# Performance work log

Hardware: AMD Instinct MI355X
Metric: run time of the kernel (lower is better)

## Reference

```python
import jax, jax.numpy as jnp
import numpy as np

N_ELEMENTS = 64  # StructureElementLayer(n_elements=64)


def setup_inputs() -> dict:
    key = jax.random.key(0)
    k1, k2 = jax.random.split(key)
    # x: [N, C, T, V] skeleton sequence (batch, coord channels, time, joints)
    x = jax.random.normal(k1, (256, 3, 256, 25), dtype=jnp.float32)
    # StructureElementLayer parameters (torch.rand init / ones*3 init)
    centres = jax.random.uniform(k2, (N_ELEMENTS, 2), dtype=jnp.float32)
    sharpness = jnp.ones((N_ELEMENTS, 2), dtype=jnp.float32) * 3.0
    return {"x": x, "centres": centres, "sharpness": sharpness}


def _mst_deaths(D):
    """Dim-0 Vietoris-Rips persistence deaths == MST edge weights (Prim's algorithm).

    D: [n, n] symmetric distance matrix. Returns [n-1] finite death values
    (births are all 0; the single essential (0, inf) pair contributes
    exp(-inf)=0 to the structure-element layer and is dropped).
    """
    n = D.shape[0]
    in_tree = jnp.zeros((n,), dtype=bool).at[0].set(True)
    dist = D[0]  # min distance from each node to the current tree

    def step(carry, _):
        in_tree, dist = carry
        d = jnp.where(in_tree, jnp.inf, dist)
        j = jnp.argmin(d)
        w = d[j]
        in_tree = in_tree.at[j].set(True)
        dist = jnp.minimum(dist, D[j])
        return (in_tree, dist), w

    (_, _), deaths = jax.lax.scan(step, (in_tree, dist), None, length=n - 1)
    return deaths


def _forward(x, centres, sharpness):
    xm = x.mean(1)                                  # [N, T, V]
    diff = xm[..., :, None] - xm[..., None, :]      # [N, T, V, V] pairwise joint diffs
    diff = diff.mean(-3)                            # [N, V, V]
    feat = jnp.linalg.norm(diff, axis=1)            # [N, V]  (torch.norm(., 2, dim=1))
    feat = (feat - feat.min()) / (feat.max() - feat.min())
    # Euclidean distance matrix of the N points in V-dim space (grad-safe sqrt)
    sq = jnp.sum(feat * feat, axis=1)
    D2 = sq[:, None] + sq[None, :] - 2.0 * (feat @ feat.T)
    D2 = jnp.maximum(D2, 0.0)
    D = jnp.where(D2 > 0.0, jnp.sqrt(jnp.where(D2 > 0.0, D2, 1.0)), 0.0)
    deaths = _mst_deaths(D)                         # [N-1]
    diag = jnp.stack([jnp.zeros_like(deaths), deaths], axis=-1)  # [N-1, 2] (birth, death)
    # StructureElementLayer: sum_i exp(-sum_d (p_id - c_kd)^2 * s_kd^2)
    d2 = (diag[:, None, :] - centres[None, :, :]) ** 2            # [N-1, K, 2]
    out = jnp.exp(-(d2 * (sharpness ** 2)).sum(-1)).sum(0)        # [K]
    return out


def reference(x, centres, sharpness):
    return _forward(x, centres, sharpness)
```

## Files before the change

### kernel.cpp

```cpp
#include <hip/hip_runtime.h>
#include <hip/hip_fp16.h>


#define WS_M    0
#define WS_MM   25600
#define WS_RK   28672
#define WS_D16  65536
#define WS_MP   196608

#define INF32 0xFFFFFFFFu
#define MPSTR 132

__global__ void k_mean(const float* __restrict__ x, float* __restrict__ m,
                       unsigned int* __restrict__ Mp) {
    const int n = blockIdx.x;
    const int tid = threadIdx.x;
    if (tid < 66) Mp[n * 66 + tid] = INF32;
    __shared__ float sums[25];
    if (tid < 25) sums[tid] = 0.0f;
    __syncthreads();
    if (tid < 200) {
        const float* base = x + (long)n * 19200 + 4 * tid;
        float a0 = 0.f, a1 = 0.f, a2 = 0.f, a3 = 0.f;
        #pragma unroll
        for (int i = 0; i < 24; ++i) {
            float4 v = *reinterpret_cast<const float4*>(base + 800 * i);
            a0 += v.x; a1 += v.y; a2 += v.z; a3 += v.w;
        }
        const int v0 = (4 * tid) % 25;
        atomicAdd(&sums[v0], a0);
        atomicAdd(&sums[(v0 + 1) % 25], a1);
        atomicAdd(&sums[(v0 + 2) % 25], a2);
        atomicAdd(&sums[(v0 + 3) % 25], a3);
    }
    __syncthreads();
    if (tid < 25) m[n * 25 + tid] = sums[tid] * (1.0f / 768.0f);
}

template <int CTRL>
__device__ __forceinline__ unsigned int dpp_min_step(unsigned int v) {
    unsigned int t = (unsigned int)__builtin_amdgcn_update_dpp(
        (int)0xFFFFFFFF, (int)v, CTRL, 0xF, 0xF, false);
    return (t < v) ? t : v;
}

__global__ void __launch_bounds__(256) k_dist(const float* __restrict__ m,
                                              unsigned short* __restrict__ D16,
                                              unsigned int* __restrict__ rowKeyG,
                                              unsigned int* __restrict__ mm) {
    __shared__ float mS[6400];
    __shared__ float featS[6400];
    __shared__ unsigned int bmin, bmax;
    __shared__ unsigned int wred[4];
    const int i = blockIdx.x;
    const int t = threadIdx.x;
    if (t == 0) { bmin = 0x7F800000u; bmax = 0u; }
    #pragma unroll
    for (int it = 0; it < 7; ++it) {
        int o = it * 256 + t;
        if (o < 1600) reinterpret_cast<float4*>(mS)[o] =
            reinterpret_cast<const float4*>(m)[o];
    }
    __syncthreads();
    float r[25];
    #pragma unroll
    for (int v = 0; v < 25; ++v) r[v] = mS[t * 25 + v];
    float S1 = 0.f, S2 = 0.f;
    #pragma unroll
    for (int v = 0; v < 25; ++v) { S1 += r[v]; S2 += r[v] * r[v]; }
    float fmn = 1e30f, fmx = -1e30f;
    #pragma unroll
    for (int w = 0; w < 25; ++w) {
        float q = S2 - 2.f * r[w] * S1 + 25.f * r[w] * r[w];
        q = fmaxf(q, 0.f);
        float f = sqrtf(q);
        featS[t * 25 + w] = f;
        fmn = fminf(fmn, f); fmx = fmaxf(fmx, f);
    }
    if (i == 0) {
        atomicMin(&bmin, __float_as_uint(fmn));
        atomicMax(&bmax, __float_as_uint(fmx));
    }
    __syncthreads();
    if (i == 0 && t == 0) { mm[0] = bmin; mm[1] = bmax; }
    float fi[25];
    #pragma unroll
    for (int v = 0; v < 25; ++v) fi[v] = featS[i * 25 + v];
    float s = 0.f;
    #pragma unroll
    for (int v = 0; v < 25; ++v) { float d = fi[v] - featS[t * 25 + v]; s += d * d; }
    const unsigned int w16 = (unsigned int)__half_as_ushort(__float2half(s));
    D16[i * 256 + t] = (unsigned short)w16;
    const unsigned int lo = (i < t) ? i : t, hi = (i < t) ? t : i;
    unsigned int key = (t == i) ? INF32 : ((w16 << 16) | (lo << 8) | hi);
    key = dpp_min_step<0x111>(key);
    key = dpp_min_step<0x112>(key);
    key = dpp_min_step<0x114>(key);
    key = dpp_min_step<0x118>(key);
    key = dpp_min_step<0x142>(key);
    key = dpp_min_step<0x143>(key);
    if ((t & 63) == 63) wred[t >> 6] = key;
    __syncthreads();
    if (t == 0) {
        unsigned int b0 = wred[0] < wred[1] ? wred[0] : wred[1];
        unsigned int b1 = wred[2] < wred[3] ? wred[2] : wred[3];
        rowKeyG[i] = b0 < b1 ? b0 : b1;
    }
}

template <bool RECORD>
__device__ __forceinline__ void wave0_phase(int n, int lane,
        unsigned int* rowKeyS, unsigned char* parentS, unsigned char* newidS,
        unsigned char* cmapS, float* deaths, unsigned int* ncS, unsigned int* dcS) {
    unsigned int par[4];
    #pragma unroll
    for (int s = 0; s < 4; ++s) {
        const int i = lane + 64 * s;
        if (i < n) {
            const unsigned int rk = rowKeyS[i];
            const unsigned int u = (rk >> 8) & 0xFFu, v = rk & 0xFFu;
            unsigned int p = (u == (unsigned int)i) ? v : u;
            if (rk == INF32) p = (unsigned int)i;
            par[s] = p;
            parentS[i] = (unsigned char)p;
        }
    }
    #pragma unroll
    for (int s = 0; s < 4; ++s) {
        const int i = lane + 64 * s;
        if (i < n) {
            const unsigned int p = par[s];
            if (p != (unsigned int)i) {
                if (parentS[p] == (unsigned char)i && (unsigned int)i < p) {
                    parentS[i] = (unsigned char)i;
                } else if (RECORD) {
                    const unsigned int d = atomicAdd(dcS, 1u);
                    const unsigned int rk = rowKeyS[i];
                    deaths[d] = sqrtf(__half2float(__ushort_as_half(
                        (unsigned short)(rk >> 16))));
                }
            }
        }
    }
    for (;;) {
        bool ch = false;
        #pragma unroll
        for (int s = 0; s < 4; ++s) {
            const int i = lane + 64 * s;
            if (i < n) {
                const unsigned char p0 = parentS[i];
                const unsigned char np = parentS[p0];
                if (np != p0) { ch = true; parentS[i] = np; }
            }
        }
        if (__ballot(ch) == 0ull) break;
    }
    bool isr[4];
    #pragma unroll
    for (int s = 0; s < 4; ++s) {
        const int i = lane + 64 * s;
        isr[s] = (i < n) && (parentS[i] == (unsigned char)i);
    }
    unsigned int base = 0;
    const unsigned long long below = (1ull << lane) - 1ull;
    #pragma unroll
    for (int s = 0; s < 4; ++s) {
        const unsigned long long mask = __ballot(isr[s]);
        if (isr[s]) {
            const int i = lane + 64 * s;
            newidS[i] = (unsigned char)(base + __popcll(mask & below));
        }
        base += (unsigned int)__popcll(mask);
    }
    if (lane == 0) *ncS = base;
    #pragma unroll
    for (int s = 0; s < 4; ++s) {
        const int i = lane + 64 * s;
        if (i < n) cmapS[i] = newidS[parentS[i]];
    }
}

__global__ void __launch_bounds__(256) k_contract(const unsigned short* __restrict__ D16g,
                                                  const unsigned int* __restrict__ rowKeyG,
                                                  unsigned int* __restrict__ Mp) {
    __shared__ unsigned int rowKeyS[256];
    __shared__ unsigned char parentS[256], newidS[256], cmapS[256];
    __shared__ unsigned int ncS;
    const int tid = threadIdx.x;
    const int b = blockIdx.x;
    rowKeyS[tid] = rowKeyG[tid];
    __syncthreads();
    if (tid < 64)
        wave0_phase<false>(256, tid, rowKeyS, parentS, newidS, cmapS,
                           nullptr, &ncS, nullptr);
    __syncthreads();
    const unsigned int ca = cmapS[b];
    const unsigned int cb = cmapS[tid];
    if (ca != cb) {
        const unsigned int w16 = (unsigned int)D16g[b * 256 + tid];
        const unsigned int lo = ca < cb ? ca : cb;
        const unsigned int hi = ca < cb ? cb : ca;
        atomicMin(&Mp[ca * MPSTR + cb], (w16 << 16) | (lo << 8) | hi);
    }
}

#define SA 132
#define SB 68
#define OFF_B (128 * SA)

__global__ void __launch_bounds__(1024) k_mst(const unsigned int* __restrict__ Mp,
                                              const unsigned int* __restrict__ rowKeyG,
                                              const unsigned int* __restrict__ mm,
                                              const float* __restrict__ centres,
                                              const float* __restrict__ sharp,
                                              float* __restrict__ out) {
    __shared__ unsigned int Mb[128 * SA + 64 * SB];
    __shared__ unsigned int rowKeyS[256];
    __shared__ unsigned char parentS[256], newidS[256], cmapS[256];
    __shared__ unsigned int ncS, dcS;
    __shared__ float deaths[256];
    __shared__ float outpart[1024];
    const int tid = threadIdx.x;

    if (tid < 256) rowKeyS[tid] = rowKeyG[tid];
    if (tid == 0) dcS = 0;
    __syncthreads();
    if (tid < 64)
        wave0_phase<true>(256, tid, rowKeyS, parentS, newidS, cmapS,
                          deaths, &ncS, &dcS);
    __syncthreads();
    int n = (int)ncS;

    for (int idx = tid; idx < n * SA; idx += 1024) Mb[idx] = Mp[idx];
    __syncthreads();

    int srcOff = 0, srcStr = SA, dstOff = OFF_B, dstStr = SB;
    for (int round = 0; round < 12 && n > 1; ++round) {
        if (tid < n) rowKeyS[tid] = INF32;
        __syncthreads();
        if (tid < 8 * n) {
            const int a = tid >> 3, sub = tid & 7;
            const unsigned int* row = &Mb[srcOff + a * srcStr];
            unsigned int best = INF32;
            for (int b2 = sub; b2 < n; b2 += 8) {
                const unsigned int v = row[b2];
                best = v < best ? v : best;
            }
            if (best != INF32) atomicMin(&rowKeyS[a], best);
        }
        __syncthreads();
        if (tid < 64)
            wave0_phase<true>(n, tid, rowKeyS, parentS, newidS, cmapS,
                              deaths, &ncS, &dcS);
        __syncthreads();
        const int nc = (int)ncS;
        if (nc > 1) {
            for (int w = tid; w < nc * dstStr; w += 1024) Mb[dstOff + w] = INF32;
            __syncthreads();
            if (tid < 8 * n) {
                const int a = tid >> 3, sub = tid & 7;
                const unsigned int ca = cmapS[a];
                const unsigned int* row = &Mb[srcOff + a * srcStr];
                for (int b2 = sub; b2 < n; b2 += 8) {
                    const unsigned int cb = cmapS[b2];
                    const unsigned int v = row[b2];
                    if (ca != cb && v != INF32) {
                        const unsigned int lo = ca < cb ? ca : cb;
                        const unsigned int hi = ca < cb ? cb : ca;
                        atomicMin(&Mb[dstOff + ca * dstStr + cb],
                                  (v & 0xFFFF0000u) | (lo << 8) | hi);
                    }
                }
            }
            __syncthreads();
        }
        const int t1 = srcOff; srcOff = dstOff; dstOff = t1;
        const int t2 = srcStr; srcStr = dstStr; dstStr = t2;
        n = nc;
    }

    const float mn = __uint_as_float(mm[0]);
    const float mx = __uint_as_float(mm[1]);
    const float inv = 1.0f / (mx - mn);
    const int k = tid & 63;
    const int part = tid >> 6;
    const float c0 = centres[2 * k], c1 = centres[2 * k + 1];
    const float s0 = sharp[2 * k],   s1 = sharp[2 * k + 1];
    const float t0 = c0 * c0 * s0 * s0;
    const float s1sq = s1 * s1;
    float acc = 0.f;
    for (int idx = part; idx < 255; idx += 16) {
        const float d = deaths[idx] * inv - c1;
        acc += __expf(-(t0 + d * d * s1sq));
    }
    outpart[tid] = acc;
    __syncthreads();
    if (tid < 64) {
        float s = 0.f;
        #pragma unroll
        for (int pp = 0; pp < 16; ++pp) s += outpart[tid + 64 * pp];
        out[tid] = s;
    }
}

extern "C" void kernel_launch(void* const* d_in, const int* in_sizes, int n_in,
                              void* d_out, int out_size, void* d_ws, size_t ws_size,
                              hipStream_t stream) {
    const float* x       = (const float*)d_in[0];
    const float* centres = (const float*)d_in[1];
    const float* sharp   = (const float*)d_in[2];
    float* out = (float*)d_out;
    char* ws = (char*)d_ws;
    float*          m   = (float*)(ws + WS_M);
    unsigned int*   mm  = (unsigned int*)(ws + WS_MM);
    unsigned int*   rk  = (unsigned int*)(ws + WS_RK);
    unsigned short* D16 = (unsigned short*)(ws + WS_D16);
    unsigned int*   Mp  = (unsigned int*)(ws + WS_MP);

    k_mean<<<256, 256, 0, stream>>>(x, m, Mp);
    k_dist<<<256, 256, 0, stream>>>(m, D16, rk, mm);
    k_contract<<<256, 256, 0, stream>>>(D16, rk, Mp);
    k_mst<<<1, 1024, 0, stream>>>(Mp, rk, mm, centres, sharp, out);
}
```

Baseline: 93.64 us.

## Fuse four kernels into one cooperative kernel with grid-wide syncs

Replaces the mean, distance, contraction and MST kernels with a single cooperative launch of 256 blocks of 1024 threads that uses grid.sync between phases. The D16 distance buffer and the min/max workspace are dropped: each block keeps its distance row in registers and block 0 reuses its own shared-memory min/max. The aim is to remove three kernel launch gaps and some global round trips. In exchange it adds grid barrier costs, leaves most threads idle in the later phases, and needs all 256 large blocks to be co-resident for the cooperative launch.

```diff
diff --git a/kernel.cpp b/kernel.cpp
--- a/kernel.cpp
+++ b/kernel.cpp
@@ -1,111 +1,26 @@
 #include <hip/hip_runtime.h>
 #include <hip/hip_fp16.h>
-
-
-#define WS_M    0
-#define WS_MM   25600
-#define WS_RK   28672
-#define WS_D16  65536
-#define WS_MP   196608
+#include <hip/hip_cooperative_groups.h>
+
+namespace cg = cooperative_groups;
+
+
+#define WS_M   0
+#define WS_RK  25600
+#define WS_MP  26624
 
 #define INF32 0xFFFFFFFFu
 #define MPSTR 132
-
-__global__ void k_mean(const float* __restrict__ x, float* __restrict__ m,
-                       unsigned int* __restrict__ Mp) {
-    const int n = blockIdx.x;
-    const int tid = threadIdx.x;
-    if (tid < 66) Mp[n * 66 + tid] = INF32;
-    __shared__ float sums[25];
-    if (tid < 25) sums[tid] = 0.0f;
-    __syncthreads();
-    if (tid < 200) {
-        const float* base = x + (long)n * 19200 + 4 * tid;
-        float a0 = 0.f, a1 = 0.f, a2 = 0.f, a3 = 0.f;
-        #pragma unroll
-        for (int i = 0; i < 24; ++i) {
-            float4 v = *reinterpret_cast<const float4*>(base + 800 * i);
-            a0 += v.x; a1 += v.y; a2 += v.z; a3 += v.w;
-        }
-        const int v0 = (4 * tid) % 25;
-        atomicAdd(&sums[v0], a0);
-        atomicAdd(&sums[(v0 + 1) % 25], a1);
-        atomicAdd(&sums[(v0 + 2) % 25], a2);
-        atomicAdd(&sums[(v0 + 3) % 25], a3);
-    }
-    __syncthreads();
-    if (tid < 25) m[n * 25 + tid] = sums[tid] * (1.0f / 768.0f);
-}
+#define SA 132
+#define SB 68
+#define OFF_B (128 * SA)
+#define POOL_BYTES 93184
 
 template <int CTRL>
 __device__ __forceinline__ unsigned int dpp_min_step(unsigned int v) {
     unsigned int t = (unsigned int)__builtin_amdgcn_update_dpp(
         (int)0xFFFFFFFF, (int)v, CTRL, 0xF, 0xF, false);
     return (t < v) ? t : v;
-}
-
-__global__ void __launch_bounds__(256) k_dist(const float* __restrict__ m,
-                                              unsigned short* __restrict__ D16,
-                                              unsigned int* __restrict__ rowKeyG,
-                                              unsigned int* __restrict__ mm) {
-    __shared__ float mS[6400];
-    __shared__ float featS[6400];
-    __shared__ unsigned int bmin, bmax;
-    __shared__ unsigned int wred[4];
-    const int i = blockIdx.x;
-    const int t = threadIdx.x;
-    if (t == 0) { bmin = 0x7F800000u; bmax = 0u; }
-    #pragma unroll
-    for (int it = 0; it < 7; ++it) {
-        int o = it * 256 + t;
-        if (o < 1600) reinterpret_cast<float4*>(mS)[o] =
-            reinterpret_cast<const float4*>(m)[o];
-    }
-    __syncthreads();
-    float r[25];
-    #pragma unroll
-    for (int v = 0; v < 25; ++v) r[v] = mS[t * 25 + v];
-    float S1 = 0.f, S2 = 0.f;
-    #pragma unroll
-    for (int v = 0; v < 25; ++v) { S1 += r[v]; S2 += r[v] * r[v]; }
-    float fmn = 1e30f, fmx = -1e30f;
-    #pragma unroll
-    for (int w = 0; w < 25; ++w) {
-        float q = S2 - 2.f * r[w] * S1 + 25.f * r[w] * r[w];
-        q = fmaxf(q, 0.f);
-        float f = sqrtf(q);
-        featS[t * 25 + w] = f;
-        fmn = fminf(fmn, f); fmx = fmaxf(fmx, f);
-    }
-    if (i == 0) {
-        atomicMin(&bmin, __float_as_uint(fmn));
-        atomicMax(&bmax, __float_as_uint(fmx));
-    }
-    __syncthreads();
-    if (i == 0 && t == 0) { mm[0] = bmin; mm[1] = bmax; }
-    float fi[25];
-    #pragma unroll
-    for (int v = 0; v < 25; ++v) fi[v] = featS[i * 25 + v];
-    float s = 0.f;
-    #pragma unroll
-    for (int v = 0; v < 25; ++v) { float d = fi[v] - featS[t * 25 + v]; s += d * d; }
-    const unsigned int w16 = (unsigned int)__half_as_ushort(__float2half(s));
-    D16[i * 256 + t] = (unsigned short)w16;
-    const unsigned int lo = (i < t) ? i : t, hi = (i < t) ? t : i;
-    unsigned int key = (t == i) ? INF32 : ((w16 << 16) | (lo << 8) | hi);
-    key = dpp_min_step<0x111>(key);
-    key = dpp_min_step<0x112>(key);
-    key = dpp_min_step<0x114>(key);
-    key = dpp_min_step<0x118>(key);
-    key = dpp_min_step<0x142>(key);
-    key = dpp_min_step<0x143>(key);
-    if ((t & 63) == 63) wred[t >> 6] = key;
-    __syncthreads();
-    if (t == 0) {
-        unsigned int b0 = wred[0] < wred[1] ? wred[0] : wred[1];
-        unsigned int b1 = wred[2] < wred[3] ? wred[2] : wred[3];
-        rowKeyG[i] = b0 < b1 ? b0 : b1;
-    }
 }
 
 template <bool RECORD>
@@ -180,51 +95,127 @@
     }
 }
 
-__global__ void __launch_bounds__(256) k_contract(const unsigned short* __restrict__ D16g,
-                                                  const unsigned int* __restrict__ rowKeyG,
-                                                  unsigned int* __restrict__ Mp) {
-    __shared__ unsigned int rowKeyS[256];
-    __shared__ unsigned char parentS[256], newidS[256], cmapS[256];
-    __shared__ unsigned int ncS;
+__global__ void __launch_bounds__(1024) k_all(const float* __restrict__ x,
+                                              const float* __restrict__ centres,
+                                              const float* __restrict__ sharp,
+                                              float* __restrict__ out,
+                                              float* __restrict__ m,
+                                              unsigned int* __restrict__ rk,
+                                              unsigned int* __restrict__ Mp) {
+    cg::grid_group grid = cg::this_grid();
+    __shared__ __align__(16) char pool[POOL_BYTES];
+    __shared__ float sums[25];
+    __shared__ unsigned int wred[4];
+    __shared__ unsigned int bminS, bmaxS, ncS, dcS;
+    __shared__ float deaths[256];
     const int tid = threadIdx.x;
     const int b = blockIdx.x;
-    rowKeyS[tid] = rowKeyG[tid];
+
+    if (tid < 66) Mp[b * 66 + tid] = INF32;
+    if (tid < 25) sums[tid] = 0.0f;
+    if (tid == 0) { bminS = 0x7F800000u; bmaxS = 0u; dcS = 0u; }
+    __syncthreads();
+    if (tid < 800) {
+        const float* base = x + (long)b * 19200 + 4 * tid;
+        float a0 = 0.f, a1 = 0.f, a2 = 0.f, a3 = 0.f;
+        #pragma unroll
+        for (int i = 0; i < 6; ++i) {
+            float4 v = *reinterpret_cast<const float4*>(base + 3200 * i);
+            a0 += v.x; a1 += v.y; a2 += v.z; a3 += v.w;
+        }
+        const int v0 = (4 * tid) % 25;
+        atomicAdd(&sums[v0], a0);
+        atomicAdd(&sums[(v0 + 1) % 25], a1);
+        atomicAdd(&sums[(v0 + 2) % 25], a2);
+        atomicAdd(&sums[(v0 + 3) % 25], a3);
+    }
+    __syncthreads();
+    if (tid < 25) m[b * 25 + tid] = sums[tid] * (1.0f / 768.0f);
+    grid.sync();
+
+    float* mS    = reinterpret_cast<float*>(pool);
+    float* featS = reinterpret_cast<float*>(pool + 25600);
+    #pragma unroll
+    for (int it = 0; it < 2; ++it) {
+        const int o = it * 1024 + tid;
+        if (o < 1600) reinterpret_cast<float4*>(mS)[o] =
+            reinterpret_cast<const float4*>(m)[o];
+    }
+    __syncthreads();
+    if (tid < 256) {
+        float r[25];
+        #pragma unroll
+        for (int v = 0; v < 25; ++v) r[v] = mS[tid * 25 + v];
+        float S1 = 0.f, S2 = 0.f;
+        #pragma unroll
+        for (int v = 0; v < 25; ++v) { S1 += r[v]; S2 += r[v] * r[v]; }
+        float fmn = 1e30f, fmx = -1e30f;
+        #pragma unroll
+        for (int w = 0; w < 25; ++w) {
+            float q = S2 - 2.f * r[w] * S1 + 25.f * r[w] * r[w];
+            q = fmaxf(q, 0.f);
+            float f = sqrtf(q);
+            featS[tid * 25 + w] = f;
+            fmn = fminf(fmn, f); fmx = fmaxf(fmx, f);
+        }
+        if (b == 0) {
+            atomicMin(&bminS, __float_as_uint(fmn));
+            atomicMax(&bmaxS, __float_as_uint(fmx));
+        }
+    }
+    __syncthreads();
+    unsigned int w16 = 0;
+    if (tid < 256) {
+        float fi[25];
+        #pragma unroll
+        for (int v = 0; v < 25; ++v) fi[v] = featS[b * 25 + v];
+        float s = 0.f;
+        #pragma unroll
+        for (int v = 0; v < 25; ++v) { float d = fi[v] - featS[tid * 25 + v]; s += d * d; }
+        w16 = (unsigned int)__half_as_ushort(__float2half(s));
+        const unsigned int lo = (b < tid) ? b : tid, hi = (b < tid) ? tid : b;
+        unsigned int key = (tid == b) ? INF32 : ((w16 << 16) | (lo << 8) | hi);
+        key = dpp_min_step<0x111>(key);
+        key = dpp_min_step<0x112>(key);
+        key = dpp_min_step<0x114>(key);
+        key = dpp_min_step<0x118>(key);
+        key = dpp_min_step<0x142>(key);
+        key = dpp_min_step<0x143>(key);
+        if ((tid & 63) == 63) wred[tid >> 6] = key;
+    }
+    __syncthreads();
+    if (tid == 0) {
+        unsigned int b0 = wred[0] < wred[1] ? wred[0] : wred[1];
+        unsigned int b1 = wred[2] < wred[3] ? wred[2] : wred[3];
+        rk[b] = b0 < b1 ? b0 : b1;
+    }
+    grid.sync();
+
+    unsigned int*  rowKeyS = reinterpret_cast<unsigned int*>(pool);
+    unsigned char* parentS = reinterpret_cast<unsigned char*>(pool + 1024);
+    unsigned char* newidS  = reinterpret_cast<unsigned char*>(pool + 1280);
+    unsigned char* cmapS   = reinterpret_cast<unsigned char*>(pool + 1536);
+    if (tid < 256) rowKeyS[tid] = rk[tid];
     __syncthreads();
     if (tid < 64)
         wave0_phase<false>(256, tid, rowKeyS, parentS, newidS, cmapS,
                            nullptr, &ncS, nullptr);
     __syncthreads();
-    const unsigned int ca = cmapS[b];
-    const unsigned int cb = cmapS[tid];
-    if (ca != cb) {
-        const unsigned int w16 = (unsigned int)D16g[b * 256 + tid];
-        const unsigned int lo = ca < cb ? ca : cb;
-        const unsigned int hi = ca < cb ? cb : ca;
-        atomicMin(&Mp[ca * MPSTR + cb], (w16 << 16) | (lo << 8) | hi);
-    }
-}
-
-#define SA 132
-#define SB 68
-#define OFF_B (128 * SA)
-
-__global__ void __launch_bounds__(1024) k_mst(const unsigned int* __restrict__ Mp,
-                                              const unsigned int* __restrict__ rowKeyG,
-                                              const unsigned int* __restrict__ mm,
-                                              const float* __restrict__ centres,
-                                              const float* __restrict__ sharp,
-                                              float* __restrict__ out) {
-    __shared__ unsigned int Mb[128 * SA + 64 * SB];
-    __shared__ unsigned int rowKeyS[256];
-    __shared__ unsigned char parentS[256], newidS[256], cmapS[256];
-    __shared__ unsigned int ncS, dcS;
-    __shared__ float deaths[256];
-    __shared__ float outpart[1024];
-    const int tid = threadIdx.x;
-
-    if (tid < 256) rowKeyS[tid] = rowKeyG[tid];
-    if (tid == 0) dcS = 0;
-    __syncthreads();
+    if (tid < 256) {
+        const unsigned int ca = cmapS[b];
+        const unsigned int cb = cmapS[tid];
+        if (ca != cb) {
+            const unsigned int lo = ca < cb ? ca : cb;
+            const unsigned int hi = ca < cb ? cb : ca;
+            atomicMin(&Mp[ca * MPSTR + cb], (w16 << 16) | (lo << 8) | hi);
+        }
+    }
+    grid.sync();
+
+    if (b != 0) return;
+    unsigned int* Mb      = reinterpret_cast<unsigned int*>(pool + 4096);
+    float*        outpart = reinterpret_cast<float*>(pool + 89088);
+
     if (tid < 64)
         wave0_phase<true>(256, tid, rowKeyS, parentS, newidS, cmapS,
                           deaths, &ncS, &dcS);
@@ -279,8 +270,8 @@
         n = nc;
     }
 
-    const float mn = __uint_as_float(mm[0]);
-    const float mx = __uint_as_float(mm[1]);
+    const float mn = __uint_as_float(bminS);
+    const float mx = __uint_as_float(bmaxS);
     const float inv = 1.0f / (mx - mn);
     const int k = tid & 63;
     const int part = tid >> 6;
@@ -311,14 +302,12 @@
     const float* sharp   = (const float*)d_in[2];
     float* out = (float*)d_out;
     char* ws = (char*)d_ws;
-    float*          m   = (float*)(ws + WS_M);
-    unsigned int*   mm  = (unsigned int*)(ws + WS_MM);
-    unsigned int*   rk  = (unsigned int*)(ws + WS_RK);
-    unsigned short* D16 = (unsigned short*)(ws + WS_D16);
-    unsigned int*   Mp  = (unsigned int*)(ws + WS_MP);
-
-    k_mean<<<256, 256, 0, stream>>>(x, m, Mp);
-    k_dist<<<256, 256, 0, stream>>>(m, D16, rk, mm);
-    k_contract<<<256, 256, 0, stream>>>(D16, rk, Mp);
-    k_mst<<<1, 1024, 0, stream>>>(Mp, rk, mm, centres, sharp, out);
+    float*        m  = (float*)(ws + WS_M);
+    unsigned int* rk = (unsigned int*)(ws + WS_RK);
+    unsigned int* Mp = (unsigned int*)(ws + WS_MP);
+
+    void* args[] = { (void*)&x, (void*)&centres, (void*)&sharp,
+                     (void*)&out, (void*)&m, (void*)&rk, (void*)&Mp };
+    hipLaunchCooperativeKernel((const void*)k_all, dim3(256), dim3(1024),
+                               args, 0, stream);
 }
```

Result: slower. 166.1 us (+77.3%).

## Fuse contraction and MST into last-block kernel, move feature computation into mean

Applied to the files above, without the earlier changes.

The edge-contraction kernel and the single-block MST kernel are merged into one launch. Each block does its contraction row, and the last block to finish, detected through a global atomic counter, runs the MST. Feature (norm) computation moves from every k_dist block into k_mean, so it is done once per sample rather than redundantly by all 256 blocks. k_mean also uses 1024 threads with fewer loads each. This removes a kernel launch and redundant compute, but all 256 blocks now allocate the large shared-memory footprint of the MST and rely on atomic ordering.

```diff
diff --git a/kernel.cpp b/kernel.cpp
--- a/kernel.cpp
+++ b/kernel.cpp
@@ -2,29 +2,33 @@
 #include <hip/hip_fp16.h>
 
 
-#define WS_M    0
+#define WS_FEAT 0
 #define WS_MM   25600
 #define WS_RK   28672
+#define WS_DONE 30720
 #define WS_D16  65536
 #define WS_MP   196608
 
 #define INF32 0xFFFFFFFFu
 #define MPSTR 132
 
-__global__ void k_mean(const float* __restrict__ x, float* __restrict__ m,
-                       unsigned int* __restrict__ Mp) {
+__global__ void __launch_bounds__(1024) k_mean(const float* __restrict__ x,
+                                               float* __restrict__ featG,
+                                               unsigned int* __restrict__ Mp,
+                                               unsigned int* __restrict__ doneG) {
     const int n = blockIdx.x;
     const int tid = threadIdx.x;
     if (tid < 66) Mp[n * 66 + tid] = INF32;
+    if (n == 0 && tid == 1023) *doneG = 0;
     __shared__ float sums[25];
     if (tid < 25) sums[tid] = 0.0f;
     __syncthreads();
-    if (tid < 200) {
+    if (tid < 800) {
         const float* base = x + (long)n * 19200 + 4 * tid;
         float a0 = 0.f, a1 = 0.f, a2 = 0.f, a3 = 0.f;
         #pragma unroll
-        for (int i = 0; i < 24; ++i) {
-            float4 v = *reinterpret_cast<const float4*>(base + 800 * i);
+        for (int i = 0; i < 6; ++i) {
+            float4 v = *reinterpret_cast<const float4*>(base + 3200 * i);
             a0 += v.x; a1 += v.y; a2 += v.z; a3 += v.w;
         }
         const int v0 = (4 * tid) % 25;
@@ -34,7 +38,18 @@
         atomicAdd(&sums[(v0 + 3) % 25], a3);
     }
     __syncthreads();
-    if (tid < 25) m[n * 25 + tid] = sums[tid] * (1.0f / 768.0f);
+    if (tid < 25) {
+        float S1 = 0.f, S2 = 0.f;
+        #pragma unroll
+        for (int v = 0; v < 25; ++v) {
+            const float rv = sums[v] * (1.0f / 768.0f);
+            S1 += rv; S2 += rv * rv;
+        }
+        const float rw = sums[tid] * (1.0f / 768.0f);
+        float q = S2 - 2.f * rw * S1 + 25.f * rw * rw;
+        q = fmaxf(q, 0.f);
+        featG[n * 25 + tid] = sqrtf(q);
+    }
 }
 
 template <int CTRL>
@@ -44,11 +59,10 @@
     return (t < v) ? t : v;
 }
 
-__global__ void __launch_bounds__(256) k_dist(const float* __restrict__ m,
+__global__ void __launch_bounds__(256) k_dist(const float* __restrict__ featG,
                                               unsigned short* __restrict__ D16,
                                               unsigned int* __restrict__ rowKeyG,
                                               unsigned int* __restrict__ mm) {
-    __shared__ float mS[6400];
     __shared__ float featS[6400];
     __shared__ unsigned int bmin, bmax;
     __shared__ unsigned int wred[4];
@@ -58,31 +72,22 @@
     #pragma unroll
     for (int it = 0; it < 7; ++it) {
         int o = it * 256 + t;
-        if (o < 1600) reinterpret_cast<float4*>(mS)[o] =
-            reinterpret_cast<const float4*>(m)[o];
-    }
-    __syncthreads();
-    float r[25];
-    #pragma unroll
-    for (int v = 0; v < 25; ++v) r[v] = mS[t * 25 + v];
-    float S1 = 0.f, S2 = 0.f;
-    #pragma unroll
-    for (int v = 0; v < 25; ++v) { S1 += r[v]; S2 += r[v] * r[v]; }
-    float fmn = 1e30f, fmx = -1e30f;
-    #pragma unroll
-    for (int w = 0; w < 25; ++w) {
-        float q = S2 - 2.f * r[w] * S1 + 25.f * r[w] * r[w];
-        q = fmaxf(q, 0.f);
-        float f = sqrtf(q);
-        featS[t * 25 + w] = f;
-        fmn = fminf(fmn, f); fmx = fmaxf(fmx, f);
-    }
+        if (o < 1600) reinterpret_cast<float4*>(featS)[o] =
+            reinterpret_cast<const float4*>(featG)[o];
+    }
+    __syncthreads();
     if (i == 0) {
+        float fmn = 1e30f, fmx = -1e30f;
+        #pragma unroll
+        for (int w = 0; w < 25; ++w) {
+            const float f = featS[t * 25 + w];
+            fmn = fminf(fmn, f); fmx = fmaxf(fmx, f);
+        }
         atomicMin(&bmin, __float_as_uint(fmn));
         atomicMax(&bmax, __float_as_uint(fmx));
-    }
-    __syncthreads();
-    if (i == 0 && t == 0) { mm[0] = bmin; mm[1] = bmax; }
+        __syncthreads();
+        if (t == 0) { mm[0] = bmin; mm[1] = bmax; }
+    }
     float fi[25];
     #pragma unroll
     for (int v = 0; v < 25; ++v) fi[v] = featS[i * 25 + v];
@@ -108,7 +113,6 @@
     }
 }
 
-template <bool RECORD>
 __device__ __forceinline__ void wave0_phase(int n, int lane,
         unsigned int* rowKeyS, unsigned char* parentS, unsigned char* newidS,
         unsigned char* cmapS, float* deaths, unsigned int* ncS, unsigned int* dcS) {
@@ -133,7 +137,7 @@
             if (p != (unsigned int)i) {
                 if (parentS[p] == (unsigned char)i && (unsigned int)i < p) {
                     parentS[i] = (unsigned char)i;
-                } else if (RECORD) {
+                } else {
                     const unsigned int d = atomicAdd(dcS, 1u);
                     const unsigned int rk = rowKeyS[i];
                     deaths[d] = sqrtf(__half2float(__ushort_as_half(
@@ -180,58 +184,58 @@
     }
 }
 
-__global__ void __launch_bounds__(256) k_contract(const unsigned short* __restrict__ D16g,
-                                                  const unsigned int* __restrict__ rowKeyG,
-                                                  unsigned int* __restrict__ Mp) {
-    __shared__ unsigned int rowKeyS[256];
-    __shared__ unsigned char parentS[256], newidS[256], cmapS[256];
-    __shared__ unsigned int ncS;
-    const int tid = threadIdx.x;
-    const int b = blockIdx.x;
-    rowKeyS[tid] = rowKeyG[tid];
-    __syncthreads();
-    if (tid < 64)
-        wave0_phase<false>(256, tid, rowKeyS, parentS, newidS, cmapS,
-                           nullptr, &ncS, nullptr);
-    __syncthreads();
-    const unsigned int ca = cmapS[b];
-    const unsigned int cb = cmapS[tid];
-    if (ca != cb) {
-        const unsigned int w16 = (unsigned int)D16g[b * 256 + tid];
-        const unsigned int lo = ca < cb ? ca : cb;
-        const unsigned int hi = ca < cb ? cb : ca;
-        atomicMin(&Mp[ca * MPSTR + cb], (w16 << 16) | (lo << 8) | hi);
-    }
-}
-
 #define SA 132
 #define SB 68
 #define OFF_B (128 * SA)
 
-__global__ void __launch_bounds__(1024) k_mst(const unsigned int* __restrict__ Mp,
-                                              const unsigned int* __restrict__ rowKeyG,
-                                              const unsigned int* __restrict__ mm,
-                                              const float* __restrict__ centres,
-                                              const float* __restrict__ sharp,
-                                              float* __restrict__ out) {
+__global__ void __launch_bounds__(1024) k_tail(const unsigned short* __restrict__ D16g,
+                                               const unsigned int* __restrict__ rowKeyG,
+                                               unsigned int* __restrict__ Mp,
+                                               unsigned int* __restrict__ doneG,
+                                               const unsigned int* __restrict__ mm,
+                                               const float* __restrict__ centres,
+                                               const float* __restrict__ sharp,
+                                               float* __restrict__ out) {
     __shared__ unsigned int Mb[128 * SA + 64 * SB];
     __shared__ unsigned int rowKeyS[256];
     __shared__ unsigned char parentS[256], newidS[256], cmapS[256];
-    __shared__ unsigned int ncS, dcS;
+    __shared__ unsigned int ncS, dcS, lastS;
     __shared__ float deaths[256];
     __shared__ float outpart[1024];
     const int tid = threadIdx.x;
+    const int b = blockIdx.x;
 
     if (tid < 256) rowKeyS[tid] = rowKeyG[tid];
     if (tid == 0) dcS = 0;
     __syncthreads();
     if (tid < 64)
-        wave0_phase<true>(256, tid, rowKeyS, parentS, newidS, cmapS,
-                          deaths, &ncS, &dcS);
-    __syncthreads();
+        wave0_phase(256, tid, rowKeyS, parentS, newidS, cmapS, deaths, &ncS, &dcS);
+    __syncthreads();
+
+    if (tid < 256) {
+        const unsigned int ca = cmapS[b];
+        const unsigned int cb = cmapS[tid];
+        if (ca != cb) {
+            const unsigned int w16 = (unsigned int)D16g[b * 256 + tid];
+            const unsigned int lo = ca < cb ? ca : cb;
+            const unsigned int hi = ca < cb ? cb : ca;
+            atomicMin(&Mp[ca * MPSTR + cb], (w16 << 16) | (lo << 8) | hi);
+        }
+    }
+    __syncthreads();
+
+    if (tid == 0) {
+        const unsigned int old = __hip_atomic_fetch_add(
+            doneG, 1u, __ATOMIC_ACQ_REL, __HIP_MEMORY_SCOPE_AGENT);
+        lastS = (old == 255u) ? 1u : 0u;
+    }
+    __syncthreads();
+    if (!lastS) return;
+
     int n = (int)ncS;
-
-    for (int idx = tid; idx < n * SA; idx += 1024) Mb[idx] = Mp[idx];
+    for (int idx = tid; idx < n * SA; idx += 1024)
+        Mb[idx] = __hip_atomic_load(&Mp[idx], __ATOMIC_RELAXED,
+                                    __HIP_MEMORY_SCOPE_AGENT);
     __syncthreads();
 
     int srcOff = 0, srcStr = SA, dstOff = OFF_B, dstStr = SB;
@@ -250,8 +254,7 @@
         }
         __syncthreads();
         if (tid < 64)
-            wave0_phase<true>(n, tid, rowKeyS, parentS, newidS, cmapS,
-                              deaths, &ncS, &dcS);
+            wave0_phase(n, tid, rowKeyS, parentS, newidS, cmapS, deaths, &ncS, &dcS);
         __syncthreads();
         const int nc = (int)ncS;
         if (nc > 1) {
@@ -311,14 +314,14 @@
     const float* sharp   = (const float*)d_in[2];
     float* out = (float*)d_out;
     char* ws = (char*)d_ws;
-    float*          m   = (float*)(ws + WS_M);
-    unsigned int*   mm  = (unsigned int*)(ws + WS_MM);
-    unsigned int*   rk  = (unsigned int*)(ws + WS_RK);
-    unsigned short* D16 = (unsigned short*)(ws + WS_D16);
-    unsigned int*   Mp  = (unsigned int*)(ws + WS_MP);
-
-    k_mean<<<256, 256, 0, stream>>>(x, m, Mp);
-    k_dist<<<256, 256, 0, stream>>>(m, D16, rk, mm);
-    k_contract<<<256, 256, 0, stream>>>(D16, rk, Mp);
-    k_mst<<<1, 1024, 0, stream>>>(Mp, rk, mm, centres, sharp, out);
-}
+    float*          featG = (float*)(ws + WS_FEAT);
+    unsigned int*   mm    = (unsigned int*)(ws + WS_MM);
+    unsigned int*   rk    = (unsigned int*)(ws + WS_RK);
+    unsigned int*   done  = (unsigned int*)(ws + WS_DONE);
+    unsigned short* D16   = (unsigned short*)(ws + WS_D16);
+    unsigned int*   Mp    = (unsigned int*)(ws + WS_MP);
+
+    k_mean<<<256, 1024, 0, stream>>>(x, featG, Mp, done);
+    k_dist<<<256, 256, 0, stream>>>(featG, D16, rk, mm);
+    k_tail<<<256, 1024, 0, stream>>>(D16, rk, Mp, done, mm, centres, sharp, out);
+}
```

Result: no change. 93.27 us (-0.4%).
